# Kernel tuning notes

Measured on AMD Instinct MI355X. Metric: run time of the kernel, lower is better.

The kernel has to match this reference:

```python
import jax, jax.numpy as jnp
import numpy as np

EPS = 1e-5

def _layernorm(x, w, b):
    mu = jnp.mean(x, axis=-1, keepdims=True)
    var = jnp.mean(jnp.square(x - mu), axis=-1, keepdims=True)
    return (x - mu) * jax.lax.rsqrt(var + EPS) * w + b

def setup_inputs() -> dict:
    key = jax.random.key(0)
    ks = jax.random.split(key, 8)
    B, N, C, D = 32, 1024, 4096, 64
    x = jax.random.normal(ks[0], (B, N, C), dtype=jnp.float32)
    gumbel = jax.random.gumbel(ks[1], (B, N, 2), dtype=jnp.float32)
    ln_w = jnp.ones((C,), jnp.float32)
    ln_b = jnp.zeros((C,), jnp.float32)
    w1 = jax.random.normal(ks[2], (C, D), dtype=jnp.float32) * 0.02
    b1 = jnp.zeros((D,), jnp.float32)
    w2 = jax.random.normal(ks[3], (D, 2), dtype=jnp.float32) * 0.02
    b2 = jnp.zeros((2,), jnp.float32)
    return {"x": x, "gumbel": gumbel, "ln_w": ln_w, "ln_b": ln_b,
            "w1": w1, "b1": b1, "w2": w2, "b2": b2}

def reference(x, gumbel, ln_w, ln_b, w1, b1, w2, b2):
    B, N, C = x.shape
    xn = _layernorm(x, ln_w, ln_b)
    local_x = xn[:, :, : C // 2]                      # [B, N, C/2]
    # policy is all-ones -> weighted mean over tokens
    global_x = jnp.mean(xn[:, :, C // 2:], axis=1, keepdims=True)  # [B, 1, C/2]
    feat = jnp.concatenate(
        [local_x, jnp.broadcast_to(global_x, local_x.shape)], axis=-1)  # [B, N, C]
    h = jax.nn.gelu(feat @ w1 + b1, approximate=False)  # [B, N, 64]
    logits = h @ w2 + b2                                # [B, N, 2]
    pred_score = jax.nn.log_softmax(logits, axis=-1)
    # gumbel-softmax (tau=1, hard=True) with straight-through estimator
    y_soft = jax.nn.softmax(pred_score + gumbel, axis=-1)
    hard = jax.nn.one_hot(jnp.argmax(y_soft, axis=-1), 2, dtype=y_soft.dtype)
    y = hard - jax.lax.stop_gradient(y_soft) + y_soft
    keep = y[:, :, 0]                                   # [B, N]
    # dense equivalent of masked_select/split: zero out dropped tokens
    return x * keep[:, :, None]
```

## Files before the change

### kernel.cpp

```cpp
#include <hip/hip_runtime.h>
#include <math.h>

#define B_   32
#define N_   1024
#define C_   4096
#define HC_  2048
#define D_   64
#define NT_  32768
#define BKC_ 128
#define NCH_ (HC_ / BKC_)
#define AST_ 68

__device__ __forceinline__ float4 ld4(const float* p) {
    return *reinterpret_cast<const float4*>(p);
}

__global__ __launch_bounds__(256) void mk1(
        const float* __restrict__ x, const float* __restrict__ lnw,
        const float* __restrict__ lnb, const float* __restrict__ w1,
        float* __restrict__ Pp, float* __restrict__ muv,
        float* __restrict__ rsv, float* __restrict__ part) {
    __shared__ float smem[16896];
    __shared__ float sLow[64], qLow[64];
    float* As = smem;
    float* Bsm = smem + 8704;

    const int t = threadIdx.x;
    const int tid = blockIdx.x;
    const int T0 = tid * 64;
    const int rt = t & 15;
    const int dt = t >> 4;
    const int row = t >> 2;
    const int fq = t & 3;
    const int lane = t & 63, w = t >> 6;

    float acc[16];
#pragma unroll
    for (int i = 0; i < 16; ++i) acc[i] = 0.f;
    float sR = 0.f, qR = 0.f;

    float4 xv[8];
    float4 wv[8];
    float lw[8];
    {
        const float* rp = x + (size_t)(T0 + row) * C_ + fq * 32;
#pragma unroll
        for (int i = 0; i < 8; ++i) xv[i] = ld4(rp + i * 4);
        const float4* s4 = reinterpret_cast<const float4*>(w1);
#pragma unroll
        for (int i = 0; i < 8; ++i) {
            wv[i] = s4[i * 256 + t];
            lw[i] = lnw[(i * 256 + t) >> 4];
        }
    }

#pragma unroll 1
    for (int c = 0; c < NCH_; ++c) {
#pragma unroll
        for (int i = 0; i < 8; ++i) {
            const float4 v = xv[i];
            const int kl = fq * 32 + i * 4;
            As[(kl + 0) * AST_ + row] = v.x;
            As[(kl + 1) * AST_ + row] = v.y;
            As[(kl + 2) * AST_ + row] = v.z;
            As[(kl + 3) * AST_ + row] = v.w;
            sR += (v.x + v.y) + (v.z + v.w);
            qR = fmaf(v.x, v.x, fmaf(v.y, v.y,
                 fmaf(v.z, v.z, fmaf(v.w, v.w, qR))));
        }
        {
            float4* b4 = reinterpret_cast<float4*>(Bsm);
#pragma unroll
            for (int i = 0; i < 8; ++i) {
                float4 v = wv[i];
                v.x *= lw[i]; v.y *= lw[i]; v.z *= lw[i]; v.w *= lw[i];
                b4[i * 256 + t] = v;
            }
        }
        __syncthreads();
        if (c + 1 < NCH_) {
            const int k1 = (c + 1) * BKC_;
            const float* rp = x + (size_t)(T0 + row) * C_ + k1 + fq * 32;
#pragma unroll
            for (int i = 0; i < 8; ++i) xv[i] = ld4(rp + i * 4);
            const float4* s4 = reinterpret_cast<const float4*>(
                w1 + (size_t)k1 * D_);
#pragma unroll
            for (int i = 0; i < 8; ++i) {
                wv[i] = s4[i * 256 + t];
                lw[i] = lnw[k1 + ((i * 256 + t) >> 4)];
            }
        }
#pragma unroll 8
        for (int k = 0; k < BKC_; ++k) {
            const float4 a4 = *reinterpret_cast<const float4*>(
                As + k * AST_ + rt * 4);
            const float4 b4 = *reinterpret_cast<const float4*>(
                Bsm + k * 64 + dt * 4);
            const float av[4] = {a4.x, a4.y, a4.z, a4.w};
            const float bv[4] = {b4.x, b4.y, b4.z, b4.w};
#pragma unroll
            for (int ri = 0; ri < 4; ++ri)
#pragma unroll
                for (int cj = 0; cj < 4; ++cj)
                    acc[ri * 4 + cj] =
                        fmaf(av[ri], bv[cj], acc[ri * 4 + cj]);
        }
        __syncthreads();
    }
#pragma unroll
    for (int ri = 0; ri < 4; ++ri) {
        float* dst = Pp + (size_t)(T0 + rt * 4 + ri) * D_ + dt * 4;
        *reinterpret_cast<float4*>(dst) = make_float4(
            acc[ri * 4 + 0], acc[ri * 4 + 1],
            acc[ri * 4 + 2], acc[ri * 4 + 3]);
    }
    sR += __shfl_xor(sR, 1); qR += __shfl_xor(qR, 1);
    sR += __shfl_xor(sR, 2); qR += __shfl_xor(qR, 2);
    if (fq == 0) { sLow[row] = sR; qLow[row] = qR; }
    __syncthreads();

    float4 wvu[8], bvu[8], gacc[8];
#pragma unroll
    for (int m = 0; m < 8; ++m) {
        wvu[m] = ld4(lnw + HC_ + (m * 64 + lane) * 4);
        bvu[m] = ld4(lnb + HC_ + (m * 64 + lane) * 4);
        gacc[m] = make_float4(0.f, 0.f, 0.f, 0.f);
    }
    for (int i = 0; i < 16; ++i) {
        const int r = w * 16 + i;
        const int tok = T0 + r;
        const float* rowp = x + (size_t)tok * C_ + HC_;
        float4 v[8];
        float s = 0.f, q = 0.f;
#pragma unroll
        for (int m = 0; m < 8; ++m) {
            v[m] = ld4(rowp + (m * 64 + lane) * 4);
            s += (v[m].x + v[m].y) + (v[m].z + v[m].w);
            q = fmaf(v[m].x, v[m].x, fmaf(v[m].y, v[m].y,
                fmaf(v[m].z, v[m].z, fmaf(v[m].w, v[m].w, q))));
        }
#pragma unroll
        for (int o = 1; o < 64; o <<= 1) {
            s += __shfl_xor(s, o);
            q += __shfl_xor(q, o);
        }
        const float S_ = s + sLow[r];
        const float Q_ = q + qLow[r];
        const float mu = S_ * (1.f / C_);
        const float rs = rsqrtf(Q_ * (1.f / C_) - mu * mu + 1e-5f);
        if (lane == 0) {
            muv[tok] = mu;
            rsv[tok] = rs;
        }
#pragma unroll
        for (int m = 0; m < 8; ++m) {
            gacc[m].x += (v[m].x - mu) * rs * wvu[m].x + bvu[m].x;
            gacc[m].y += (v[m].y - mu) * rs * wvu[m].y + bvu[m].y;
            gacc[m].z += (v[m].z - mu) * rs * wvu[m].z + bvu[m].z;
            gacc[m].w += (v[m].w - mu) * rs * wvu[m].w + bvu[m].w;
        }
    }
    float (*sh)[HC_] = reinterpret_cast<float(*)[HC_]>(smem);
    __syncthreads();
#pragma unroll
    for (int m = 0; m < 8; ++m)
        *reinterpret_cast<float4*>(&sh[w][(m * 64 + lane) * 4]) = gacc[m];
    __syncthreads();
    float* pp = part + (size_t)tid * HC_;
#pragma unroll
    for (int m = 0; m < 8; ++m) {
        const int j = (m * 64 + lane) * 4;
        const float4 a0 = ld4(&sh[0][j]);
        const float4 a1 = ld4(&sh[1][j]);
        const float4 a2 = ld4(&sh[2][j]);
        const float4 a3 = ld4(&sh[3][j]);
        float4 r;
        r.x = (a0.x + a1.x) + (a2.x + a3.x);
        r.y = (a0.y + a1.y) + (a2.y + a3.y);
        r.z = (a0.z + a1.z) + (a2.z + a3.z);
        r.w = (a0.w + a1.w) + (a2.w + a3.w);
        if (w == (m & 3))
            *reinterpret_cast<float4*>(pp + j) = r;
    }
}

__global__ __launch_bounds__(256) void k2a_part(
        const float* __restrict__ part, const float* __restrict__ w1,
        const float* __restrict__ lnw, const float* __restrict__ lnb,
        float* __restrict__ gpart, float* __restrict__ Wpart,
        float* __restrict__ Bpart) {
    __shared__ float Gs[256];
    __shared__ float red[512];
    const int t = threadIdx.x;
    const int d = t & 63, s = t >> 6;
    const int blk = blockIdx.x;
    if (blk < 256) {
        const int b = blk >> 3, jq = blk & 7;
        const int j = jq * 256 + t;
        float a = 0.f;
        for (int k = 0; k < 16; ++k)
            a += part[(size_t)(b * 16 + k) * HC_ + j];
        Gs[t] = a;
        __syncthreads();
        float acc = 0.f;
        const int j0 = jq * 256 + s * 64;
        for (int jj = 0; jj < 64; ++jj)
            acc = fmaf(Gs[s * 64 + jj],
                       w1[(size_t)(HC_ + j0 + jj) * D_ + d], acc);
        red[s * 64 + d] = acc;
        __syncthreads();
        if (s == 0)
            gpart[(size_t)blk * 64 + d] =
                red[d] + red[64 + d] + red[128 + d] + red[192 + d];
    } else {
        const int wq = blk - 256;
        const int c0 = wq * 256 + s * 64;
        float a = 0.f, c2 = 0.f;
        for (int c = c0; c < c0 + 64; ++c) {
            const float wvv = w1[(size_t)c * D_ + d];
            a = fmaf(lnw[c], wvv, a);
            c2 = fmaf(lnb[c], wvv, c2);
        }
        red[s * 64 + d] = a;
        red[256 + s * 64 + d] = c2;
        __syncthreads();
        if (s == 0) {
            Wpart[wq * 64 + d] =
                red[d] + red[64 + d] + red[128 + d] + red[192 + d];
            Bpart[wq * 64 + d] = red[256 + d] + red[320 + d]
                               + red[384 + d] + red[448 + d];
        }
    }
}

__global__ __launch_bounds__(256) void k45_decide_mask(
        const float* __restrict__ Pp, const float* __restrict__ muv,
        const float* __restrict__ rsv, const float* __restrict__ gpart,
        const float* __restrict__ Wpart, const float* __restrict__ Bpart,
        const float* __restrict__ b1, const float* __restrict__ w2,
        const float* __restrict__ b2, const float* __restrict__ gum,
        const float* __restrict__ x, float* __restrict__ out) {
    const int t = threadIdx.x;
    const int lane = t & 63, w = t >> 6;
    const int token = blockIdx.x * 4 + w;
    const int b = token >> 10;

    float W1 = 0.f, Bsv = 0.f, gt = 0.f;
#pragma unroll
    for (int q = 0; q < 8; ++q) {
        W1 += Wpart[q * 64 + lane];
        Bsv += Bpart[q * 64 + lane];
        gt += gpart[(size_t)(b * 8 + q) * 64 + lane];
    }
    gt *= (1.f / N_);

    const float2 gv = *reinterpret_cast<const float2*>(gum + token * 2);
    const float p = Pp[(size_t)token * D_ + lane];
    const float mu = muv[token], rs = rsv[token];
    float h = rs * (p - mu * W1) + Bsv + gt + b1[lane];
    h = 0.5f * h * (1.f + erff(h * 0.70710678118654752f));
    const float2 w2v = *reinterpret_cast<const float2*>(w2 + lane * 2);
    float l0 = h * w2v.x;
    float l1 = h * w2v.y;
#pragma unroll
    for (int o = 1; o < 64; o <<= 1) {
        l0 += __shfl_xor(l0, o);
        l1 += __shfl_xor(l1, o);
    }
    const float z0 = l0 + b2[0] + gv.x;
    const float z1 = l1 + b2[1] + gv.y;

    float4* dst = reinterpret_cast<float4*>(out + (size_t)token * C_);
    if (z0 >= z1) {
        const float4* src =
            reinterpret_cast<const float4*>(x + (size_t)token * C_);
#pragma unroll
        for (int c = 0; c < 16; ++c)
            dst[c * 64 + lane] = src[c * 64 + lane];
    } else {
        const float4 z = make_float4(0.f, 0.f, 0.f, 0.f);
#pragma unroll
        for (int c = 0; c < 16; ++c)
            dst[c * 64 + lane] = z;
    }
}

extern "C" void kernel_launch(void* const* d_in, const int* in_sizes, int n_in,
                              void* d_out, int out_size, void* d_ws,
                              size_t ws_size, hipStream_t stream) {
    const float* x   = (const float*)d_in[0];
    const float* gum = (const float*)d_in[1];
    const float* lnw = (const float*)d_in[2];
    const float* lnb = (const float*)d_in[3];
    const float* w1  = (const float*)d_in[4];
    const float* b1  = (const float*)d_in[5];
    const float* w2  = (const float*)d_in[6];
    const float* b2  = (const float*)d_in[7];
    float* out = (float*)d_out;

    float* wsf   = (float*)d_ws;
    float* Pp    = wsf;
    float* muv   = Pp + (size_t)NT_ * D_;
    float* rsv   = muv + NT_;
    float* part  = rsv + NT_;
    float* gpart = part + (size_t)512 * HC_;
    float* Wpart = gpart + 256 * 64;
    float* Bpart = Wpart + 8 * 64;

    mk1<<<512, 256, 0, stream>>>(x, lnw, lnb, w1, Pp, muv, rsv, part);
    k2a_part<<<264, 256, 0, stream>>>(part, w1, lnw, lnb,
                                      gpart, Wpart, Bpart);
    k45_decide_mask<<<NT_ / 4, 256, 0, stream>>>(Pp, muv, rsv, gpart,
                                                 Wpart, Bpart, b1, w2, b2,
                                                 gum, x, out);
}
```

Before: 361.0 us.

## Split K across warps with 8x8 register tiles and reduce partial sums in LDS

The per-thread GEMM tile grows from 4x4 to 8x8 and the K dimension is split across the four waves, each handling 32 of the 128 k-values per chunk. The four per-wave partial 64x64 results are then written to shared memory and summed before the store to Pp. The aim is fewer LDS reads per FMA and more arithmetic intensity per thread. The cost is 64 accumulator registers, which may reduce occupancy, plus an extra LDS reduction step and a barrier.

```diff
diff --git a/kernel.cpp b/kernel.cpp
--- a/kernel.cpp
+++ b/kernel.cpp
@@ -28,15 +28,14 @@
     const int t = threadIdx.x;
     const int tid = blockIdx.x;
     const int T0 = tid * 64;
-    const int rt = t & 15;
-    const int dt = t >> 4;
     const int row = t >> 2;
     const int fq = t & 3;
     const int lane = t & 63, w = t >> 6;
-
-    float acc[16];
-#pragma unroll
-    for (int i = 0; i < 16; ++i) acc[i] = 0.f;
+    const int rt = lane >> 3, dt = lane & 7;
+
+    float acc[64];
+#pragma unroll
+    for (int i = 0; i < 64; ++i) acc[i] = 0.f;
     float sR = 0.f, qR = 0.f;
 
     float4 xv[8];
@@ -92,32 +91,54 @@
             }
         }
 #pragma unroll 8
-        for (int k = 0; k < BKC_; ++k) {
-            const float4 a4 = *reinterpret_cast<const float4*>(
-                As + k * AST_ + rt * 4);
-            const float4 b4 = *reinterpret_cast<const float4*>(
-                Bsm + k * 64 + dt * 4);
-            const float av[4] = {a4.x, a4.y, a4.z, a4.w};
-            const float bv[4] = {b4.x, b4.y, b4.z, b4.w};
-#pragma unroll
-            for (int ri = 0; ri < 4; ++ri)
-#pragma unroll
-                for (int cj = 0; cj < 4; ++cj)
-                    acc[ri * 4 + cj] =
-                        fmaf(av[ri], bv[cj], acc[ri * 4 + cj]);
-        }
-        __syncthreads();
-    }
-#pragma unroll
-    for (int ri = 0; ri < 4; ++ri) {
-        float* dst = Pp + (size_t)(T0 + rt * 4 + ri) * D_ + dt * 4;
-        *reinterpret_cast<float4*>(dst) = make_float4(
-            acc[ri * 4 + 0], acc[ri * 4 + 1],
-            acc[ri * 4 + 2], acc[ri * 4 + 3]);
+        for (int kk = 0; kk < 32; ++kk) {
+            const int k = w * 32 + kk;
+            const float4 a0 = *reinterpret_cast<const float4*>(
+                As + k * AST_ + rt * 8);
+            const float4 a1 = *reinterpret_cast<const float4*>(
+                As + k * AST_ + rt * 8 + 4);
+            const float4 b0 = *reinterpret_cast<const float4*>(
+                Bsm + k * 64 + dt * 8);
+            const float4 b1 = *reinterpret_cast<const float4*>(
+                Bsm + k * 64 + dt * 8 + 4);
+            const float av[8] = {a0.x, a0.y, a0.z, a0.w,
+                                 a1.x, a1.y, a1.z, a1.w};
+            const float bv[8] = {b0.x, b0.y, b0.z, b0.w,
+                                 b1.x, b1.y, b1.z, b1.w};
+#pragma unroll
+            for (int ri = 0; ri < 8; ++ri)
+#pragma unroll
+                for (int cj = 0; cj < 8; ++cj)
+                    acc[ri * 8 + cj] =
+                        fmaf(av[ri], bv[cj], acc[ri * 8 + cj]);
+        }
+        __syncthreads();
     }
     sR += __shfl_xor(sR, 1); qR += __shfl_xor(qR, 1);
     sR += __shfl_xor(sR, 2); qR += __shfl_xor(qR, 2);
     if (fq == 0) { sLow[row] = sR; qLow[row] = qR; }
+
+#pragma unroll
+    for (int i = 0; i < 64; ++i) smem[i * 256 + t] = acc[i];
+    __syncthreads();
+#pragma unroll
+    for (int r2 = 0; r2 < 2; ++r2) {
+        const int rowO = rt * 8 + w * 2 + r2;
+        float v[8];
+#pragma unroll
+        for (int cj = 0; cj < 8; ++cj) {
+            const int i = w * 16 + r2 * 8 + cj;
+            v[cj] = (smem[i * 256 + lane]
+                     + smem[i * 256 + 64 + lane])
+                  + (smem[i * 256 + 128 + lane]
+                     + smem[i * 256 + 192 + lane]);
+        }
+        float* dst = Pp + (size_t)(T0 + rowO) * D_ + dt * 8;
+        *reinterpret_cast<float4*>(dst) =
+            make_float4(v[0], v[1], v[2], v[3]);
+        *reinterpret_cast<float4*>(dst + 4) =
+            make_float4(v[4], v[5], v[6], v[7]);
+    }
     __syncthreads();
 
     float4 wvu[8], bvu[8], gacc[8];
```

After: 352.6 us (median of 2 runs). -2.3%, faster.
